# Performance work log

Hardware: AMD Instinct MI355X
Metric: run time of the kernel (lower is better)

Reference implementation:

```python
import jax, jax.numpy as jnp
import numpy as np
import math

HEAD_DIM = 64

def setup_inputs() -> dict:
    key = jax.random.key(0)
    kq, kk, kv, km = jax.random.split(key, 4)
    B, H, S, D = 4, 16, 2048, HEAD_DIM
    Q = jax.random.normal(kq, (B, H, S, D), dtype=jnp.float32)
    K = jax.random.normal(kk, (B, H, S, D), dtype=jnp.float32)
    V = jax.random.normal(kv, (B, H, S, D), dtype=jnp.float32)
    mask = jax.random.randint(km, (B, S), 0, 2, dtype=jnp.int32)
    return {"Q": Q, "K": K, "V": V, "mask": mask}

def reference(Q, K, V, mask):
    # dot: [B, H, S, S]
    scale = 1.0 / math.sqrt(HEAD_DIM)
    dot = jnp.einsum("bhsd,bhtd->bhst", Q, K) * scale
    # additive mask: subtract 1e6 where mask == 0 (mask broadcast over heads and query pos)
    m = mask.astype(dot.dtype)[:, None, None, :]  # [B, 1, 1, S]
    dot = dot - 1000000.0 * (1.0 - m)
    attn = jax.nn.softmax(dot, axis=-1)
    # dropout_prob = 0.0 (eval / deterministic), so dropout is identity
    X = jnp.einsum("bhst,bhtd->bhsd", attn, V)
    return X
```

## Files before the change

### kernel.cpp

```cpp
#include <hip/hip_runtime.h>

#define S_LEN 2048
#define HD 64
#define KVB 64

typedef float f32x4  __attribute__((ext_vector_type(4)));
typedef float f32x16 __attribute__((ext_vector_type(16)));
typedef short bf16x8 __attribute__((ext_vector_type(8)));
typedef int   i32x4  __attribute__((ext_vector_type(4)));

#define SQ_SCALE 0.18033688011112042f
#define MASK_B  (-1442695.040888963f)
#define THR 10.0f

static __device__ __forceinline__ int cvt_pk(float lo, float hi) {
  int r;
  asm("v_cvt_pk_bf16_f32 %0, %1, %2" : "=v"(r) : "v"(lo), "v"(hi));
  return r;
}
static __device__ __forceinline__ float exp2v(float x) {
  float r;
  asm("v_exp_f32 %0, %1" : "=v"(r) : "v"(x));
  return r;
}
static __device__ __forceinline__ void swap32(int &a, int &b) {
  asm("v_permlane32_swap_b32 %0, %1" : "+v"(a), "+v"(b));
}

__global__ __launch_bounds__(256)
void build_idx(const int* __restrict__ Mg, int* __restrict__ idxA,
               float* __restrict__ biasA, int* __restrict__ cntA) {
  const int b    = threadIdx.x >> 6;
  const int lane = threadIdx.x & 63;
  const int* m   = Mg + (size_t)b * S_LEN;
  int*   idx  = idxA  + (size_t)b * S_LEN;
  float* bias = biasA + (size_t)b * S_LEN;

  int offset = 0;
  for (int kb = 0; kb < S_LEN; kb += 64) {
    int live = (m[kb + lane] != 0);
    unsigned long long bal = __ballot(live);
    unsigned long long lt  = (1ull << lane) - 1ull;
    int pos = offset + (int)__popcll(bal & lt);
    if (live) idx[pos] = kb + lane;
    offset += (int)__popcll(bal);
  }
  const int cnt = offset;
  for (int j = lane; j < S_LEN; j += 64) {
    bias[j] = (j < cnt) ? 0.f : MASK_B;
    if (j >= cnt) idx[j] = 0;
  }
  if (lane == 0) cntA[b] = (cnt + 63) & ~63;
}

__global__ __launch_bounds__(512, 4)
void attn_fwd(const float* __restrict__ Qg, const float* __restrict__ Kg,
              const float* __restrict__ Vg,
              const int* __restrict__ idxA, const float* __restrict__ biasA,
              const int* __restrict__ cntA, float* __restrict__ Og) {
  __shared__ __align__(16) short Klds[2][64 * 72];
  __shared__ __align__(16) short Vtld[2][64 * 72];
  __shared__ __align__(16) float MB[2][64];

  const int t    = threadIdx.x;
  const int lane = t & 63;
  const int wid  = t >> 6;
  const int c    = lane & 31;
  const int hi   = lane >> 5;

  const int bid  = (int)blockIdx.x;
  const int swz  = (bid & 7) * 64 + (bid >> 3);
  const int bh   = swz >> 3;
  const int qblk = (swz & 7) * 256;
  const int b    = bh >> 4;
  const size_t base = (size_t)bh * S_LEN * HD;
  const int qbase = qblk + wid * 32;

  const int*   idx  = idxA  + (size_t)b * S_LEN;
  const float* bias = biasA + (size_t)b * S_LEN;
  const int NTd = cntA[b] >> 6;

  bf16x8 qf[4];
#pragma unroll
  for (int s = 0; s < 4; ++s) {
    const float* qp = Qg + base + (size_t)(qbase + c) * HD + 16*s + 8*hi;
    float4 x0 = *(const float4*)qp;
    float4 x1 = *(const float4*)(qp + 4);
    i32x4 w;
    w[0] = cvt_pk(x0.x*SQ_SCALE, x0.y*SQ_SCALE);
    w[1] = cvt_pk(x0.z*SQ_SCALE, x0.w*SQ_SCALE);
    w[2] = cvt_pk(x1.x*SQ_SCALE, x1.y*SQ_SCALE);
    w[3] = cvt_pk(x1.z*SQ_SCALE, x1.w*SQ_SCALE);
    qf[s] = __builtin_bit_cast(bf16x8, w);
  }

  const int kkey = t >> 3;
  const int kdg  = (t & 7) ^ (kkey & 7);
  const int vd   = t & 63;
  const int vkg  = t >> 6;

  float kr[8], vr[8]; float mbias = 0.f;

  auto LOADT = [&](int it) {
    const int tb = it * KVB;
    const int krow = idx[tb + kkey];
    const float* kp = Kg + base + (size_t)krow * HD + 8*kdg;
    *(float4*)&kr[0] = *(const float4*)kp;
    *(float4*)&kr[4] = *(const float4*)(kp + 4);
    i32x4 ra = *(const i32x4*)&idx[tb + 8*vkg];
    i32x4 rb = *(const i32x4*)&idx[tb + 8*vkg + 4];
#pragma unroll
    for (int j = 0; j < 4; ++j) vr[j]   = Vg[base + (size_t)ra[j]*HD + vd];
#pragma unroll
    for (int j = 0; j < 4; ++j) vr[4+j] = Vg[base + (size_t)rb[j]*HD + vd];
    if (t < 64) mbias = bias[tb + t];
  };
  auto STORET = [&](int bf) {
    i32x4 kw;
    kw[0] = cvt_pk(kr[0], kr[1]); kw[1] = cvt_pk(kr[2], kr[3]);
    kw[2] = cvt_pk(kr[4], kr[5]); kw[3] = cvt_pk(kr[6], kr[7]);
    *(i32x4*)&Klds[bf][kkey*72 + 8*kdg] = kw;
    i32x4 vw;
    vw[0] = cvt_pk(vr[0], vr[1]); vw[1] = cvt_pk(vr[2], vr[3]);
    vw[2] = cvt_pk(vr[4], vr[5]); vw[3] = cvt_pk(vr[6], vr[7]);
    *(i32x4*)&Vtld[bf][vd*72 + 8*vkg] = vw;
    if (t < 64) MB[bf][t] = mbias;
  };

  f32x16 acc0 = {};
  f32x16 acc1 = {};
  float mrun = -1e30f;
  float lrun = 0.f;

  auto GROUP = [&](int cur, int grp, bool lastTile) {
    const int kc = 32 * grp;
    f32x16 S = {};
    __builtin_amdgcn_s_setprio(1);
#pragma unroll
    for (int s = 0; s < 4; ++s) {
      bf16x8 kf = *(const bf16x8*)&Klds[cur][(kc + c)*72 + 16*s + 8*hi];
      S = __builtin_amdgcn_mfma_f32_32x32x16_bf16(kf, qf[s], S, 0, 0, 0);
    }
    __builtin_amdgcn_s_setprio(0);

    float sb[16];
    if (lastTile) {
      f32x4 b4[4];
#pragma unroll
      for (int m = 0; m < 4; ++m)
        b4[m] = *(const f32x4*)&MB[cur][kc + 8*m + 4*hi];
#pragma unroll
      for (int r = 0; r < 16; ++r)
        sb[r] = S[r] + b4[r >> 2][r & 3];
    } else {
#pragma unroll
      for (int r = 0; r < 16; ++r) sb[r] = S[r];
    }

    float mx[8];
#pragma unroll
    for (int r = 0; r < 8; ++r) mx[r] = fmaxf(sb[r], sb[r+8]);
#pragma unroll
    for (int r = 0; r < 4; ++r) mx[r] = fmaxf(mx[r], mx[r+4]);
    float tmax = fmaxf(fmaxf(mx[0], mx[1]), fmaxf(mx[2], mx[3]));
    tmax = fmaxf(tmax, __shfl_xor(tmax, 32, 64));

    if (!__all(tmax <= mrun + THR)) {
      float mnew = fmaxf(mrun, tmax);
      float al = exp2v(mrun - mnew);
      acc0 *= al; acc1 *= al;
      lrun *= al; mrun = mnew;
    }

    float p0[8], p1[8];
#pragma unroll
    for (int r = 0; r < 8; ++r) p0[r] = exp2v(sb[r] - mrun);
#pragma unroll
    for (int r = 0; r < 8; ++r) p1[r] = exp2v(sb[8 + r] - mrun);

    int w0 = cvt_pk(p0[0], p0[1]), w1 = cvt_pk(p0[2], p0[3]);
    int w2 = cvt_pk(p0[4], p0[5]), w3 = cvt_pk(p0[6], p0[7]);
    swap32(w0, w2); swap32(w1, w3);
    i32x4 pq0 = {w0, w1, w2, w3};
    bf16x8 pb0 = __builtin_bit_cast(bf16x8, pq0);
    int w4 = cvt_pk(p1[0], p1[1]), w5 = cvt_pk(p1[2], p1[3]);
    int w6 = cvt_pk(p1[4], p1[5]), w7 = cvt_pk(p1[6], p1[7]);
    swap32(w4, w6); swap32(w5, w7);
    i32x4 pq1 = {w4, w5, w6, w7};
    bf16x8 pb1 = __builtin_bit_cast(bf16x8, pq1);

    bf16x8 vA0 = *(const bf16x8*)&Vtld[cur][(c     )*72 + kc      + 8*hi];
    bf16x8 vA1 = *(const bf16x8*)&Vtld[cur][(c     )*72 + kc + 16 + 8*hi];
    bf16x8 vB0 = *(const bf16x8*)&Vtld[cur][(c + 32)*72 + kc      + 8*hi];
    bf16x8 vB1 = *(const bf16x8*)&Vtld[cur][(c + 32)*72 + kc + 16 + 8*hi];

    __builtin_amdgcn_s_setprio(1);
    acc0 = __builtin_amdgcn_mfma_f32_32x32x16_bf16(vA0, pb0, acc0, 0, 0, 0);
    acc1 = __builtin_amdgcn_mfma_f32_32x32x16_bf16(vB0, pb0, acc1, 0, 0, 0);
    acc0 = __builtin_amdgcn_mfma_f32_32x32x16_bf16(vA1, pb1, acc0, 0, 0, 0);
    acc1 = __builtin_amdgcn_mfma_f32_32x32x16_bf16(vB1, pb1, acc1, 0, 0, 0);
    __builtin_amdgcn_s_setprio(0);

    float s0 = ((p0[0]+p0[1]) + (p0[2]+p0[3])) + ((p0[4]+p0[5]) + (p0[6]+p0[7]));
    float s1 = ((p1[0]+p1[1]) + (p1[2]+p1[3])) + ((p1[4]+p1[5]) + (p1[6]+p1[7]));
    lrun += s0 + s1;
  };

  LOADT(0); STORET(0);
  if (NTd > 1) LOADT(1);
  __syncthreads();

  for (int it = 0; it < NTd; ++it) {
    if (it + 1 < NTd) STORET((it + 1) & 1);
    if (it + 2 < NTd) LOADT(it + 2);
    const int cur = it & 1;
    const bool lt = (it == NTd - 1);
    GROUP(cur, 0, lt);
    GROUP(cur, 1, lt);
    __syncthreads();
  }

  float lfull = lrun + __shfl_xor(lrun, 32, 64);
  const float linv = 1.0f / lfull;
  float* op = Og + base + (size_t)(qbase + c) * HD + 4*hi;
#pragma unroll
  for (int m = 0; m < 4; ++m) {
    f32x4 o0, o1;
#pragma unroll
    for (int j = 0; j < 4; ++j) {
      o0[j] = acc0[4*m + j] * linv;
      o1[j] = acc1[4*m + j] * linv;
    }
    *(f32x4*)(op + 8*m)      = o0;
    *(f32x4*)(op + 32 + 8*m) = o1;
  }
}

extern "C" void kernel_launch(void* const* d_in, const int* in_sizes, int n_in,
                              void* d_out, int out_size, void* d_ws, size_t ws_size,
                              hipStream_t stream) {
    const float* Q = (const float*)d_in[0];
    const float* K = (const float*)d_in[1];
    const float* V = (const float*)d_in[2];
    const int*   M = (const int*)d_in[3];
    float* O = (float*)d_out;

    char* ws = (char*)d_ws;
    int*   idxA  = (int*)ws;
    float* biasA = (float*)(ws + 4 * S_LEN * sizeof(int));
    int*   cntA  = (int*)(ws + 8 * S_LEN * sizeof(int));

    hipLaunchKernelGGL(build_idx, dim3(1), dim3(256), 0, stream, M, idxA, biasA, cntA);
    hipLaunchKernelGGL(attn_fwd, dim3(512), dim3(512), 0, stream,
                       Q, K, V, idxA, biasA, cntA, O);
}
```

Baseline: 76.87 us.

## Process 64-key tiles in one softmax step and double the barrier interval

```diff
diff --git a/kernel.cpp b/kernel.cpp
--- a/kernel.cpp
+++ b/kernel.cpp
@@ -58,9 +58,9 @@
               const float* __restrict__ Vg,
               const int* __restrict__ idxA, const float* __restrict__ biasA,
               const int* __restrict__ cntA, float* __restrict__ Og) {
-  __shared__ __align__(16) short Klds[2][64 * 72];
-  __shared__ __align__(16) short Vtld[2][64 * 72];
-  __shared__ __align__(16) float MB[2][64];
+  __shared__ __align__(16) short Klds[4][64 * 72];
+  __shared__ __align__(16) short Vtld[4][64 * 72];
+  __shared__ __align__(16) float MB[4][64];
 
   const int t    = threadIdx.x;
   const int lane = t & 63;
@@ -132,34 +132,37 @@
   float mrun = -1e30f;
   float lrun = 0.f;
 
-  auto GROUP = [&](int cur, int grp, bool lastTile) {
-    const int kc = 32 * grp;
-    f32x16 S = {};
+  auto COMPUTE = [&](int cur, bool lastTile) {
+    f32x16 S0 = {}, S1 = {};
     __builtin_amdgcn_s_setprio(1);
 #pragma unroll
     for (int s = 0; s < 4; ++s) {
-      bf16x8 kf = *(const bf16x8*)&Klds[cur][(kc + c)*72 + 16*s + 8*hi];
-      S = __builtin_amdgcn_mfma_f32_32x32x16_bf16(kf, qf[s], S, 0, 0, 0);
+      bf16x8 kf0 = *(const bf16x8*)&Klds[cur][(c     )*72 + 16*s + 8*hi];
+      bf16x8 kf1 = *(const bf16x8*)&Klds[cur][(c + 32)*72 + 16*s + 8*hi];
+      S0 = __builtin_amdgcn_mfma_f32_32x32x16_bf16(kf0, qf[s], S0, 0, 0, 0);
+      S1 = __builtin_amdgcn_mfma_f32_32x32x16_bf16(kf1, qf[s], S1, 0, 0, 0);
     }
     __builtin_amdgcn_s_setprio(0);
 
-    float sb[16];
+    float l0[16], l1[16];
     if (lastTile) {
-      f32x4 b4[4];
-#pragma unroll
-      for (int m = 0; m < 4; ++m)
-        b4[m] = *(const f32x4*)&MB[cur][kc + 8*m + 4*hi];
-#pragma unroll
-      for (int r = 0; r < 16; ++r)
-        sb[r] = S[r] + b4[r >> 2][r & 3];
+      f32x4 b4[8];
+#pragma unroll
+      for (int m = 0; m < 8; ++m)
+        b4[m] = *(const f32x4*)&MB[cur][8*m + 4*hi];
+#pragma unroll
+      for (int r = 0; r < 16; ++r) l0[r] = S0[r] + b4[r >> 2][r & 3];
+#pragma unroll
+      for (int r = 0; r < 16; ++r) l1[r] = S1[r] + b4[4 + (r >> 2)][r & 3];
     } else {
 #pragma unroll
-      for (int r = 0; r < 16; ++r) sb[r] = S[r];
+      for (int r = 0; r < 16; ++r) { l0[r] = S0[r]; l1[r] = S1[r]; }
     }
 
     float mx[8];
 #pragma unroll
-    for (int r = 0; r < 8; ++r) mx[r] = fmaxf(sb[r], sb[r+8]);
+    for (int r = 0; r < 8; ++r)
+      mx[r] = fmaxf(fmaxf(l0[r], l0[r+8]), fmaxf(l1[r], l1[r+8]));
 #pragma unroll
     for (int r = 0; r < 4; ++r) mx[r] = fmaxf(mx[r], mx[r+4]);
     float tmax = fmaxf(fmaxf(mx[0], mx[1]), fmaxf(mx[2], mx[3]));
@@ -172,51 +175,79 @@
       lrun *= al; mrun = mnew;
     }
 
-    float p0[8], p1[8];
-#pragma unroll
-    for (int r = 0; r < 8; ++r) p0[r] = exp2v(sb[r] - mrun);
-#pragma unroll
-    for (int r = 0; r < 8; ++r) p1[r] = exp2v(sb[8 + r] - mrun);
-
-    int w0 = cvt_pk(p0[0], p0[1]), w1 = cvt_pk(p0[2], p0[3]);
-    int w2 = cvt_pk(p0[4], p0[5]), w3 = cvt_pk(p0[6], p0[7]);
-    swap32(w0, w2); swap32(w1, w3);
-    i32x4 pq0 = {w0, w1, w2, w3};
-    bf16x8 pb0 = __builtin_bit_cast(bf16x8, pq0);
-    int w4 = cvt_pk(p1[0], p1[1]), w5 = cvt_pk(p1[2], p1[3]);
-    int w6 = cvt_pk(p1[4], p1[5]), w7 = cvt_pk(p1[6], p1[7]);
-    swap32(w4, w6); swap32(w5, w7);
-    i32x4 pq1 = {w4, w5, w6, w7};
-    bf16x8 pb1 = __builtin_bit_cast(bf16x8, pq1);
-
-    bf16x8 vA0 = *(const bf16x8*)&Vtld[cur][(c     )*72 + kc      + 8*hi];
-    bf16x8 vA1 = *(const bf16x8*)&Vtld[cur][(c     )*72 + kc + 16 + 8*hi];
-    bf16x8 vB0 = *(const bf16x8*)&Vtld[cur][(c + 32)*72 + kc      + 8*hi];
-    bf16x8 vB1 = *(const bf16x8*)&Vtld[cur][(c + 32)*72 + kc + 16 + 8*hi];
-
-    __builtin_amdgcn_s_setprio(1);
-    acc0 = __builtin_amdgcn_mfma_f32_32x32x16_bf16(vA0, pb0, acc0, 0, 0, 0);
-    acc1 = __builtin_amdgcn_mfma_f32_32x32x16_bf16(vB0, pb0, acc1, 0, 0, 0);
-    acc0 = __builtin_amdgcn_mfma_f32_32x32x16_bf16(vA1, pb1, acc0, 0, 0, 0);
-    acc1 = __builtin_amdgcn_mfma_f32_32x32x16_bf16(vB1, pb1, acc1, 0, 0, 0);
-    __builtin_amdgcn_s_setprio(0);
-
-    float s0 = ((p0[0]+p0[1]) + (p0[2]+p0[3])) + ((p0[4]+p0[5]) + (p0[6]+p0[7]));
-    float s1 = ((p1[0]+p1[1]) + (p1[2]+p1[3])) + ((p1[4]+p1[5]) + (p1[6]+p1[7]));
-    lrun += s0 + s1;
+    float p0[16];
+#pragma unroll
+    for (int r = 0; r < 16; ++r) p0[r] = exp2v(l0[r] - mrun);
+    {
+      int w0 = cvt_pk(p0[0], p0[1]), w1 = cvt_pk(p0[2], p0[3]);
+      int w2 = cvt_pk(p0[4], p0[5]), w3 = cvt_pk(p0[6], p0[7]);
+      swap32(w0, w2); swap32(w1, w3);
+      i32x4 pq0 = {w0, w1, w2, w3};
+      bf16x8 pb0 = __builtin_bit_cast(bf16x8, pq0);
+      int w4 = cvt_pk(p0[8], p0[9]),  w5 = cvt_pk(p0[10], p0[11]);
+      int w6 = cvt_pk(p0[12], p0[13]), w7 = cvt_pk(p0[14], p0[15]);
+      swap32(w4, w6); swap32(w5, w7);
+      i32x4 pq1 = {w4, w5, w6, w7};
+      bf16x8 pb1 = __builtin_bit_cast(bf16x8, pq1);
+
+      bf16x8 vA0 = *(const bf16x8*)&Vtld[cur][(c     )*72      + 8*hi];
+      bf16x8 vB0 = *(const bf16x8*)&Vtld[cur][(c + 32)*72      + 8*hi];
+      bf16x8 vA1 = *(const bf16x8*)&Vtld[cur][(c     )*72 + 16 + 8*hi];
+      bf16x8 vB1 = *(const bf16x8*)&Vtld[cur][(c + 32)*72 + 16 + 8*hi];
+      __builtin_amdgcn_s_setprio(1);
+      acc0 = __builtin_amdgcn_mfma_f32_32x32x16_bf16(vA0, pb0, acc0, 0, 0, 0);
+      acc1 = __builtin_amdgcn_mfma_f32_32x32x16_bf16(vB0, pb0, acc1, 0, 0, 0);
+      acc0 = __builtin_amdgcn_mfma_f32_32x32x16_bf16(vA1, pb1, acc0, 0, 0, 0);
+      acc1 = __builtin_amdgcn_mfma_f32_32x32x16_bf16(vB1, pb1, acc1, 0, 0, 0);
+      __builtin_amdgcn_s_setprio(0);
+      float s0 = ((p0[0]+p0[1]) + (p0[2]+p0[3])) + ((p0[4]+p0[5]) + (p0[6]+p0[7]));
+      float s1 = ((p0[8]+p0[9]) + (p0[10]+p0[11])) + ((p0[12]+p0[13]) + (p0[14]+p0[15]));
+      lrun += s0 + s1;
+    }
+
+    float p1[16];
+#pragma unroll
+    for (int r = 0; r < 16; ++r) p1[r] = exp2v(l1[r] - mrun);
+    {
+      int w0 = cvt_pk(p1[0], p1[1]), w1 = cvt_pk(p1[2], p1[3]);
+      int w2 = cvt_pk(p1[4], p1[5]), w3 = cvt_pk(p1[6], p1[7]);
+      swap32(w0, w2); swap32(w1, w3);
+      i32x4 pq2 = {w0, w1, w2, w3};
+      bf16x8 pb2 = __builtin_bit_cast(bf16x8, pq2);
+      int w4 = cvt_pk(p1[8], p1[9]),  w5 = cvt_pk(p1[10], p1[11]);
+      int w6 = cvt_pk(p1[12], p1[13]), w7 = cvt_pk(p1[14], p1[15]);
+      swap32(w4, w6); swap32(w5, w7);
+      i32x4 pq3 = {w4, w5, w6, w7};
+      bf16x8 pb3 = __builtin_bit_cast(bf16x8, pq3);
+
+      bf16x8 vA2 = *(const bf16x8*)&Vtld[cur][(c     )*72 + 32 + 8*hi];
+      bf16x8 vB2 = *(const bf16x8*)&Vtld[cur][(c + 32)*72 + 32 + 8*hi];
+      bf16x8 vA3 = *(const bf16x8*)&Vtld[cur][(c     )*72 + 48 + 8*hi];
+      bf16x8 vB3 = *(const bf16x8*)&Vtld[cur][(c + 32)*72 + 48 + 8*hi];
+      __builtin_amdgcn_s_setprio(1);
+      acc0 = __builtin_amdgcn_mfma_f32_32x32x16_bf16(vA2, pb2, acc0, 0, 0, 0);
+      acc1 = __builtin_amdgcn_mfma_f32_32x32x16_bf16(vB2, pb2, acc1, 0, 0, 0);
+      acc0 = __builtin_amdgcn_mfma_f32_32x32x16_bf16(vA3, pb3, acc0, 0, 0, 0);
+      acc1 = __builtin_amdgcn_mfma_f32_32x32x16_bf16(vB3, pb3, acc1, 0, 0, 0);
+      __builtin_amdgcn_s_setprio(0);
+      float s0 = ((p1[0]+p1[1]) + (p1[2]+p1[3])) + ((p1[4]+p1[5]) + (p1[6]+p1[7]));
+      float s1 = ((p1[8]+p1[9]) + (p1[10]+p1[11])) + ((p1[12]+p1[13]) + (p1[14]+p1[15]));
+      lrun += s0 + s1;
+    }
   };
 
   LOADT(0); STORET(0);
-  if (NTd > 1) LOADT(1);
+  if (NTd > 1) { LOADT(1); STORET(1); }
+  if (NTd > 2) LOADT(2);
   __syncthreads();
 
-  for (int it = 0; it < NTd; ++it) {
-    if (it + 1 < NTd) STORET((it + 1) & 1);
-    if (it + 2 < NTd) LOADT(it + 2);
-    const int cur = it & 1;
-    const bool lt = (it == NTd - 1);
-    GROUP(cur, 0, lt);
-    GROUP(cur, 1, lt);
+  for (int it = 0; it < NTd; it += 2) {
+    if (it + 2 < NTd) STORET((it + 2) & 3);
+    if (it + 3 < NTd) LOADT(it + 3);
+    COMPUTE(it & 3, it == NTd - 1);
+    if (it + 3 < NTd) STORET((it + 3) & 3);
+    if (it + 4 < NTd) LOADT(it + 4);
+    if (it + 1 < NTd) COMPUTE((it + 1) & 3, it + 1 == NTd - 1);
     __syncthreads();
   }
 
```

After: 130.6 us. 69.9% more time.
